# Kernel tuning notes

Measured on AMD Instinct MI355X. Metric: run time of the kernel, lower is better.

Reference implementation:

```python
import jax, jax.numpy as jnp
import numpy as np

C = 128

def setup_inputs() -> dict:
    key = jax.random.key(0)
    ks = jax.random.split(key, 7)
    s = 1.0 / np.sqrt(C)
    return {
        "x": jax.random.normal(ks[0], (8, C, 64, 64), dtype=jnp.float32),
        "Wq": jax.random.uniform(ks[1], (C, C), jnp.float32, -s, s),
        "bq": jax.random.uniform(ks[2], (C,), jnp.float32, -s, s),
        "Wk": jax.random.uniform(ks[3], (C, C), jnp.float32, -s, s),
        "bk": jax.random.uniform(ks[4], (C,), jnp.float32, -s, s),
        "Wv": jax.random.uniform(ks[5], (C, C), jnp.float32, -s, s),
        "bv": jax.random.uniform(ks[6], (C,), jnp.float32, -s, s),
    }

def reference(x, Wq, bq, Wk, bk, Wv, bv):
    bs, c, h, w = x.shape
    xf = x.reshape(bs, c, h * w)                      # [B, C, N]
    # 1x1 convs == per-pixel linear maps over channels
    q = jnp.einsum("dc,bcn->bdn", Wq, xf) + bq[None, :, None]
    k = jnp.einsum("dc,bcn->bdn", Wk, xf) + bk[None, :, None]
    v = jnp.einsum("dc,bcn->bdn", Wv, xf) + bv[None, :, None]
    # energy[b,i,j] = <q[:,i], k[:,j]>  (no 1/sqrt(d) scaling, per original)
    energy = jnp.einsum("bci,bcj->bij", q, k)         # [B, N, N]
    attn = jax.nn.softmax(energy, axis=-1)
    # out[b,c,i] = sum_j v[b,c,j] * attn[b,i,j]
    out = jnp.einsum("bcj,bij->bci", v, attn)
    return out.reshape(bs, c, h, w)
```

## Files before the change

### kernel.cpp

```cpp
#include <hip/hip_runtime.h>
#include <stdint.h>
#include <math.h>

typedef float  f32x4  __attribute__((ext_vector_type(4)));
typedef float  f32x16 __attribute__((ext_vector_type(16)));
typedef short  bf16x8 __attribute__((ext_vector_type(8)));
typedef unsigned int u32;
typedef unsigned int u32x4 __attribute__((ext_vector_type(4)));
typedef unsigned short ushort_t;

#define MFMA32(a, b, c) __builtin_amdgcn_mfma_f32_32x32x16_bf16((a), (b), (c), 0, 0, 0)

constexpr int B_ = 8, C_ = 128, N_ = 4096;
constexpr float LOG2E = 1.44269504088896340736f;

__device__ __forceinline__ u32 pack2bf(float a, float b) {
  u32 ua = __builtin_bit_cast(u32, a);
  u32 ub = __builtin_bit_cast(u32, b);
  ua += 0x7fffu + ((ua >> 16) & 1u);
  ub += 0x7fffu + ((ub >> 16) & 1u);
  return (ua >> 16) | (ub & 0xffff0000u);
}
__device__ __forceinline__ u32 pkfast(float a, float b) {
  u32 ua = __builtin_bit_cast(u32, a) + 0x8000u;
  u32 ub = __builtin_bit_cast(u32, b) + 0x8000u;
  return __builtin_amdgcn_perm(ub, ua, 0x07060302u);
}
__device__ __forceinline__ bf16x8 pack8(const float* v, float s) {
  u32x4 d = { pack2bf(v[0]*s, v[1]*s), pack2bf(v[2]*s, v[3]*s),
              pack2bf(v[4]*s, v[5]*s), pack2bf(v[6]*s, v[7]*s) };
  return __builtin_bit_cast(bf16x8, d);
}

__device__ __forceinline__ void gload_lds16(const ushort_t* g, ushort_t* l) {
  __builtin_amdgcn_global_load_lds(
      (const __attribute__((address_space(1))) void*)g,
      (__attribute__((address_space(3))) void*)l, 16, 0, 0);
}

__device__ __forceinline__ bf16x8 mk_pa(const f32x16& sv, int rb, float& lacc,
                                        int lq1) {
  float e0 = __builtin_amdgcn_exp2f(sv[rb+0]);
  float e1 = __builtin_amdgcn_exp2f(sv[rb+1]);
  float e2 = __builtin_amdgcn_exp2f(sv[rb+2]);
  float e3 = __builtin_amdgcn_exp2f(sv[rb+3]);
  float e4 = __builtin_amdgcn_exp2f(sv[rb+4]);
  float e5 = __builtin_amdgcn_exp2f(sv[rb+5]);
  float e6 = __builtin_amdgcn_exp2f(sv[rb+6]);
  float e7 = __builtin_amdgcn_exp2f(sv[rb+7]);
  lacc += ((e0+e1)+(e2+e3)) + ((e4+e5)+(e6+e7));
  u32 a  = pkfast(e0, e1), b2 = pkfast(e2, e3);
  u32 c2 = pkfast(e4, e5), d2 = pkfast(e6, e7);
  u32 s0v = lq1 ? a : c2;
  u32 s1v = lq1 ? b2 : d2;
  u32 r0 = __shfl_xor(s0v, 32);
  u32 r1 = __shfl_xor(s1v, 32);
  u32x4 fr;
  fr[0] = lq1 ? r0 : a;
  fr[1] = lq1 ? r1 : b2;
  fr[2] = lq1 ? c2 : r0;
  fr[3] = lq1 ? d2 : r1;
  return __builtin_bit_cast(bf16x8, fr);
}

__global__ __launch_bounds__(256)
void wprep_kernel(const float* __restrict__ Wq, const float* __restrict__ Wk,
                  const float* __restrict__ Wv, ushort_t* __restrict__ Wf)
{
  const int tid  = blockIdx.x * 256 + threadIdx.x;
  const int widx = tid >> 11;
  const int r    = tid & 2047;
  const int dt   = r >> 9;
  const int kc   = (r >> 6) & 7;
  const int ln   = r & 63;
  const float* W = (widx == 0) ? Wq : (widx == 1) ? Wk : Wv;
  const float s  = (widx == 0) ? LOG2E : 1.0f;
  const int d    = dt * 32 + (ln & 31);
  const int c0   = kc * 16 + (ln >> 5) * 8;
  const float* p = W + d * C_ + c0;
  f32x4 lo = *(const f32x4*)p, hi = *(const f32x4*)(p + 4);
  float v[8] = { lo.x, lo.y, lo.z, lo.w, hi.x, hi.y, hi.z, hi.w };
  *(bf16x8*)(Wf + (size_t)tid * 8) = pack8(v, s);
}

__global__ __launch_bounds__(256, 3)
void proj_kernel(const float* __restrict__ x,
                 const float* __restrict__ bq, const float* __restrict__ bk,
                 const float* __restrict__ bv, const ushort_t* __restrict__ Wf,
                 ushort_t* __restrict__ Qf, ushort_t* __restrict__ Kf,
                 ushort_t* __restrict__ Vf)
{
  const int b   = blockIdx.x & 7;
  const int nt  = blockIdx.x >> 3;
  const int n0  = nt << 5;
  const int t   = threadIdx.x;
  const int dt  = t >> 6;
  const int lane = t & 63;
  const int l31 = t & 31;
  const int lq1 = (t >> 5) & 1;

  __shared__ float xs[128 * 33];
  {
    const float* xb = x + (size_t)b * C_ * N_ + n0;
    const int m  = t & 7;
    const int cb = t >> 3;
#pragma unroll
    for (int it = 0; it < 4; ++it) {
      const int c = it * 32 + cb;
      f32x4 v = *(const f32x4*)(xb + (size_t)c * N_ + m * 4);
      *(f32x4*)&xs[c * 33 + m * 4] = v;
    }
  }
  __syncthreads();

  bf16x8 xf[8];
#pragma unroll
  for (int kc = 0; kc < 8; ++kc) {
    float v[8];
#pragma unroll
    for (int e = 0; e < 8; ++e)
      v[e] = xs[(kc * 16 + lq1 * 8 + e) * 33 + l31];
    xf[kc] = pack8(v, 1.0f);
  }

  const ushort_t* WQf = Wf;
  const ushort_t* WKf = Wf + 16384;
  const ushort_t* WVf = Wf + 32768;
  const f32x16 Z = {0,0,0,0,0,0,0,0,0,0,0,0,0,0,0,0};

  f32x16 sq = Z, sk = Z, sv = Z;
#pragma unroll
  for (int kc = 0; kc < 8; ++kc) {
    const size_t wo = (size_t)(dt * 8 + kc) * 512 + lane * 8;
    bf16x8 wq = *(const bf16x8*)(WQf + wo);
    bf16x8 wk = *(const bf16x8*)(WKf + wo);
    bf16x8 wvv = *(const bf16x8*)(WVf + wo);
    sq = MFMA32(wq, xf[kc], sq);
    sk = MFMA32(wk, xf[kc], sk);
    sv = MFMA32(xf[kc], wvv, sv);
  }

#pragma unroll
  for (int q = 0; q < 4; ++q) {
    const int dbase = dt * 32 + q * 8 + lq1 * 4;
    f32x4 b4q = *(const f32x4*)(bq + dbase);
    f32x4 b4k = *(const f32x4*)(bk + dbase);
    uint2 qs, ks;
    qs.x = pack2bf(sq[4*q+0] + b4q.x * LOG2E, sq[4*q+1] + b4q.y * LOG2E);
    qs.y = pack2bf(sq[4*q+2] + b4q.z * LOG2E, sq[4*q+3] + b4q.w * LOG2E);
    ks.x = pack2bf(sk[4*q+0] + b4k.x, sk[4*q+1] + b4k.y);
    ks.y = pack2bf(sk[4*q+2] + b4k.z, sk[4*q+3] + b4k.w);
    const int kcf = dt * 2 + (q >> 1), h = q & 1;
    const size_t off = ((size_t)((b * 128 + nt) * 8 + kcf) * 64 + h * 32 + l31) * 8 + lq1 * 4;
    *(uint2*)(Qf + off) = qs;
    *(uint2*)(Kf + off) = ks;
  }

  {
    const float bvl = bv[dt * 32 + l31];
    const int j64 = nt >> 1, qp = nt & 1;
#pragma unroll
    for (int q = 0; q < 4; ++q) {
      uint2 vs;
      vs.x = pack2bf(sv[4*q+0] + bvl, sv[4*q+1] + bvl);
      vs.y = pack2bf(sv[4*q+2] + bvl, sv[4*q+3] + bvl);
      const int cc = qp * 2 + (q >> 1);
      const size_t off = ((size_t)((b * 64 + j64) * 4 + dt) * 4 + cc) * 512 +
                         (size_t)((q & 1) * 32 + l31) * 8 + lq1 * 4;
      *(uint2*)(Vf + off) = vs;
    }
  }
}

__global__ __launch_bounds__(256, 3)
void flash_kernel(const ushort_t* __restrict__ Qf, const ushort_t* __restrict__ Kf,
                  const ushort_t* __restrict__ Vf, float* __restrict__ out,
                  float* __restrict__ opart, float* __restrict__ lpart, int js)
{
  const int b     = blockIdx.x & 7;
  const int itile = (blockIdx.x >> 3) & 31;
  const int jsl   = blockIdx.x >> 8;
  const int t     = threadIdx.x;
  const int wv    = t >> 6;
  const int lane  = t & 63;
  const int l31   = t & 31;
  const int lq1   = (t >> 5) & 1;
  const int i0    = itile * 128 + wv * 32;

  __shared__ __align__(16) short smem[16384];

  const int jt0 = (jsl * 128) / js;
  const int jt1 = ((jsl + 1) * 128) / js;
  const ushort_t* Kt0   = Kf + (size_t)b * 524288;
  const ushort_t* Vbase = Vf + (size_t)b * 524288;

  auto stage = [&](int jt, int p) {
    ushort_t* buf = (ushort_t*)smem + p * 8192;
    if (wv < 2) {
      const ushort_t* src = Kt0 + (size_t)jt * 4096;
#pragma unroll
      for (int c = 0; c < 4; ++c) {
        const int g = wv * 4 + c;
        gload_lds16(src + g * 512 + lane * 8, buf + g * 512);
      }
    } else {
      const int qp = jt & 1;
      const ushort_t* src = Vbase + (size_t)(jt >> 1) * 8192;
#pragma unroll
      for (int c = 0; c < 4; ++c) {
        const int h2 = (wv - 2) * 4 + c;
        const int ct = h2 >> 1, h = h2 & 1;
        gload_lds16(src + (size_t)(ct * 4 + qp * 2 + h) * 512 + lane * 8,
                    buf + 4096 + h2 * 512);
      }
    }
  };

  bf16x8 qf[8];
  const size_t qb = (size_t)((b * 128 + itile * 4 + wv) * 8) * 512;
#pragma unroll
  for (int kc = 0; kc < 8; ++kc)
    qf[kc] = *(const bf16x8*)(Qf + qb + (size_t)kc * 512 + lane * 8);

  const f32x16 Z = {0,0,0,0,0,0,0,0,0,0,0,0,0,0,0,0};
  f32x16 o[4] = {Z, Z, Z, Z};
  float lsum = 0.f;

  stage(jt0, 0);
  __syncthreads();

  for (int jt = jt0; jt < jt1; ++jt) {
    const int par = (jt - jt0) & 1;
    if (jt + 1 < jt1) stage(jt + 1, par ^ 1);

    const short* kbuf = smem + par * 8192;
    const short* vbuf = kbuf + 4096;

    f32x16 s = Z;
#pragma unroll
    for (int kc = 0; kc < 8; ++kc) {
      bf16x8 kf = *(const bf16x8*)&kbuf[kc * 512 + lane * 8];
      s = MFMA32(kf, qf[kc], s);
    }
    bf16x8 pa0 = mk_pa(s, 0, lsum, lq1);
    bf16x8 pa1 = mk_pa(s, 8, lsum, lq1);
#pragma unroll
    for (int ct = 0; ct < 4; ++ct) {
      bf16x8 vf0 = *(const bf16x8*)&vbuf[(ct * 2 + 0) * 512 + lane * 8];
      o[ct] = MFMA32(vf0, pa0, o[ct]);
      bf16x8 vf1 = *(const bf16x8*)&vbuf[(ct * 2 + 1) * 512 + lane * 8];
      o[ct] = MFMA32(vf1, pa1, o[ct]);
    }
    __syncthreads();
  }

  lsum += __shfl_xor(lsum, 32);
  const int ib = i0 + l31;

  if (js == 1) {
    const float inv = 1.0f / lsum;
#pragma unroll
    for (int ct = 0; ct < 4; ++ct)
#pragma unroll
      for (int rg = 0; rg < 16; ++rg) {
        const int c = ct * 32 + (rg >> 2) * 8 + lq1 * 4 + (rg & 3);
        out[(size_t)(b * C_ + c) * N_ + ib] = o[ct][rg] * inv;
      }
  } else {
    float* op = jsl ? (opart + (size_t)(jsl - 1) * B_ * C_ * N_) : out;
#pragma unroll
    for (int ct = 0; ct < 4; ++ct)
#pragma unroll
      for (int rg = 0; rg < 16; ++rg) {
        const int c = ct * 32 + (rg >> 2) * 8 + lq1 * 4 + (rg & 3);
        op[(size_t)(b * C_ + c) * N_ + ib] = o[ct][rg];
      }
    if (lane < 32)
      lpart[(size_t)jsl * B_ * N_ + (size_t)b * N_ + ib] = lsum;
  }
}

__global__ __launch_bounds__(256)
void combine_kernel(const float* __restrict__ opart, const float* __restrict__ lpart,
                    float* __restrict__ out, int js)
{
  const int t  = blockIdx.x * 256 + threadIdx.x;
  const int n4 = (t & 1023) * 4;
  const int bc = t >> 10;
  const int b  = bc >> 7;
  const size_t off  = (size_t)bc * N_ + n4;
  const size_t loff = (size_t)b * N_ + n4;
  f32x4 os = *(const f32x4*)(out + off);
  f32x4 ls = *(const f32x4*)(lpart + loff);
  for (int s = 1; s < js; ++s) {
    os += *(const f32x4*)(opart + (size_t)(s - 1) * B_ * C_ * N_ + off);
    ls += *(const f32x4*)(lpart + (size_t)s * B_ * N_ + loff);
  }
  f32x4 r = { os.x / ls.x, os.y / ls.y, os.z / ls.z, os.w / ls.w };
  *(f32x4*)(out + off) = r;
}

extern "C" void kernel_launch(void* const* d_in, const int* in_sizes, int n_in,
                              void* d_out, int out_size, void* d_ws, size_t ws_size,
                              hipStream_t stream) {
  const float* x  = (const float*)d_in[0];
  const float* Wq = (const float*)d_in[1];
  const float* bq = (const float*)d_in[2];
  const float* Wk = (const float*)d_in[3];
  const float* bk = (const float*)d_in[4];
  const float* Wv = (const float*)d_in[5];
  const float* bv = (const float*)d_in[6];
  float* out = (float*)d_out;

  const size_t nc = (size_t)B_ * N_ * C_;
  ushort_t* qf = (ushort_t*)d_ws;
  ushort_t* kf = qf + nc;
  ushort_t* vf = kf + nc;
  ushort_t* wf = vf + nc;
  const size_t base = (3 * nc + 49152) * sizeof(ushort_t);

  auto need = [&](int jss) {
    return base + (size_t)jss * (size_t)B_ * N_ * 4 +
           (size_t)(jss - 1) * (size_t)B_ * C_ * N_ * 4;
  };
  const int js = (ws_size >= need(3)) ? 3 : (ws_size >= need(2)) ? 2 : 1;

  float* lpart = (float*)((char*)d_ws + base);
  float* opart = lpart + (size_t)js * B_ * N_;

  hipLaunchKernelGGL(wprep_kernel, dim3(24), dim3(256), 0, stream, Wq, Wk, Wv, wf);
  hipLaunchKernelGGL(proj_kernel, dim3(1024), dim3(256), 0, stream,
                     x, bq, bk, bv, wf, qf, kf, vf);
  hipLaunchKernelGGL(flash_kernel, dim3(256 * js), dim3(256), 0, stream,
                     qf, kf, vf, out, opart, lpart, js);
  if (js > 1)
    hipLaunchKernelGGL(combine_kernel, dim3(4096), dim3(256), 0, stream,
                       opart, lpart, out, js);
}
```

Measured before the change: 173.9 us.

## Software-pipeline QK and PV across tiles with split K/V staging

Splits K and V staging into separate double buffers and restructures the main loop so the QK^T MFMAs for tile n+1 are issued alongside the PV MFMAs for tile n. The softmax exponentiation (mk_pa) then runs after both MFMA groups, so its VALU work can overlap with matrix-core work rather than sitting on the critical path between dependent MFMAs. It also raises wave priority around the MFMA block. In exchange it adds a prologue and epilogue, keeps more live registers (s plus pa0/pa1 across iterations), and staggers the K and V buffer indices in a way that must stay correct for every split count.

```diff
diff --git a/kernel.cpp b/kernel.cpp
--- a/kernel.cpp
+++ b/kernel.cpp
@@ -191,19 +191,24 @@
 
   const int jt0 = (jsl * 128) / js;
   const int jt1 = ((jsl + 1) * 128) / js;
+  const int NT  = jt1 - jt0;
   const ushort_t* Kt0   = Kf + (size_t)b * 524288;
   const ushort_t* Vbase = Vf + (size_t)b * 524288;
 
-  auto stage = [&](int jt, int p) {
-    ushort_t* buf = (ushort_t*)smem + p * 8192;
+  auto stageK = [&](int jt, int p) {
     if (wv < 2) {
+      ushort_t* buf = (ushort_t*)smem + p * 4096;
       const ushort_t* src = Kt0 + (size_t)jt * 4096;
 #pragma unroll
       for (int c = 0; c < 4; ++c) {
         const int g = wv * 4 + c;
         gload_lds16(src + g * 512 + lane * 8, buf + g * 512);
       }
-    } else {
+    }
+  };
+  auto stageV = [&](int jt, int p) {
+    if (wv >= 2) {
+      ushort_t* buf = (ushort_t*)smem + 8192 + p * 4096;
       const int qp = jt & 1;
       const ushort_t* src = Vbase + (size_t)(jt >> 1) * 8192;
 #pragma unroll
@@ -211,7 +216,7 @@
         const int h2 = (wv - 2) * 4 + c;
         const int ct = h2 >> 1, h = h2 & 1;
         gload_lds16(src + (size_t)(ct * 4 + qp * 2 + h) * 512 + lane * 8,
-                    buf + 4096 + h2 * 512);
+                    buf + h2 * 512);
       }
     }
   };
@@ -226,32 +231,51 @@
   f32x16 o[4] = {Z, Z, Z, Z};
   float lsum = 0.f;
 
-  stage(jt0, 0);
-  __syncthreads();
-
-  for (int jt = jt0; jt < jt1; ++jt) {
-    const int par = (jt - jt0) & 1;
-    if (jt + 1 < jt1) stage(jt + 1, par ^ 1);
-
-    const short* kbuf = smem + par * 8192;
-    const short* vbuf = kbuf + 4096;
-
+  auto qk = [&](const short* kbuf) -> f32x16 {
     f32x16 s = Z;
 #pragma unroll
     for (int kc = 0; kc < 8; ++kc) {
-      bf16x8 kf = *(const bf16x8*)&kbuf[kc * 512 + lane * 8];
-      s = MFMA32(kf, qf[kc], s);
-    }
-    bf16x8 pa0 = mk_pa(s, 0, lsum, lq1);
-    bf16x8 pa1 = mk_pa(s, 8, lsum, lq1);
+      bf16x8 kfr = *(const bf16x8*)&kbuf[kc * 512 + lane * 8];
+      s = MFMA32(kfr, qf[kc], s);
+    }
+    return s;
+  };
+  auto pv = [&](const short* vbuf, bf16x8 a0, bf16x8 a1) {
 #pragma unroll
     for (int ct = 0; ct < 4; ++ct) {
       bf16x8 vf0 = *(const bf16x8*)&vbuf[(ct * 2 + 0) * 512 + lane * 8];
-      o[ct] = MFMA32(vf0, pa0, o[ct]);
+      o[ct] = MFMA32(vf0, a0, o[ct]);
       bf16x8 vf1 = *(const bf16x8*)&vbuf[(ct * 2 + 1) * 512 + lane * 8];
-      o[ct] = MFMA32(vf1, pa1, o[ct]);
-    }
+      o[ct] = MFMA32(vf1, a1, o[ct]);
+    }
+  };
+
+  stageK(jt0, 0);
+  stageV(jt0, 0);
+  __syncthreads();
+  if (NT > 1) stageK(jt0 + 1, 1);
+  f32x16 s0 = qk(smem);
+  bf16x8 pa0 = mk_pa(s0, 0, lsum, lq1);
+  bf16x8 pa1 = mk_pa(s0, 8, lsum, lq1);
+  __syncthreads();
+
+  for (int n = 0; n < NT - 1; ++n) {
+    if (n + 2 < NT) stageK(jt0 + n + 2, n & 1);
+    stageV(jt0 + n + 1, (n + 1) & 1);
+    const short* kb = smem + ((n + 1) & 1) * 4096;
+    const short* vb = smem + 8192 + (n & 1) * 4096;
+    __builtin_amdgcn_s_setprio(1);
+    f32x16 s = qk(kb);
+    pv(vb, pa0, pa1);
+    __builtin_amdgcn_s_setprio(0);
+    pa0 = mk_pa(s, 0, lsum, lq1);
+    pa1 = mk_pa(s, 8, lsum, lq1);
     __syncthreads();
+  }
+
+  {
+    const short* vb = smem + 8192 + ((NT - 1) & 1) * 4096;
+    pv(vb, pa0, pa1);
   }
 
   lsum += __shfl_xor(lsum, 32);
```

After: 172.7 us. About the same (-0.7%).

## Triple-buffer K/V staging with all waves loading and explicit vmcnt waits

Applied to the files above, without the earlier changes.

Moves K/V LDS staging from double to triple buffering, keeping two tiles in flight ahead of compute. All four waves now share both K and V loads instead of splitting K to two waves and V to the other two. The full __syncthreads is replaced by a partial s_waitcnt vmcnt plus a raw s_barrier, so later loads stay outstanding across the barrier. MFMA sections are also wrapped in s_setprio. LDS use grows from 32KB to 48KB per block, which may limit the 3-blocks-per-CU occupancy target.

```diff
diff --git a/kernel.cpp b/kernel.cpp
--- a/kernel.cpp
+++ b/kernel.cpp
@@ -187,32 +187,31 @@
   const int lq1   = (t >> 5) & 1;
   const int i0    = itile * 128 + wv * 32;
 
-  __shared__ __align__(16) short smem[16384];
+  __shared__ __align__(16) short smem[24576];
 
   const int jt0 = (jsl * 128) / js;
   const int jt1 = ((jsl + 1) * 128) / js;
+  const int NT  = jt1 - jt0;
   const ushort_t* Kt0   = Kf + (size_t)b * 524288;
   const ushort_t* Vbase = Vf + (size_t)b * 524288;
 
   auto stage = [&](int jt, int p) {
-    ushort_t* buf = (ushort_t*)smem + p * 8192;
-    if (wv < 2) {
-      const ushort_t* src = Kt0 + (size_t)jt * 4096;
-#pragma unroll
-      for (int c = 0; c < 4; ++c) {
-        const int g = wv * 4 + c;
-        gload_lds16(src + g * 512 + lane * 8, buf + g * 512);
-      }
-    } else {
-      const int qp = jt & 1;
-      const ushort_t* src = Vbase + (size_t)(jt >> 1) * 8192;
-#pragma unroll
-      for (int c = 0; c < 4; ++c) {
-        const int h2 = (wv - 2) * 4 + c;
-        const int ct = h2 >> 1, h = h2 & 1;
-        gload_lds16(src + (size_t)(ct * 4 + qp * 2 + h) * 512 + lane * 8,
-                    buf + 4096 + h2 * 512);
-      }
+    ushort_t* kb = (ushort_t*)smem + p * 4096;
+    ushort_t* vb = (ushort_t*)smem + 12288 + p * 4096;
+    const ushort_t* ksrc = Kt0 + (size_t)jt * 4096;
+    const int qp = jt & 1;
+    const ushort_t* vsrc = Vbase + (size_t)(jt >> 1) * 8192;
+#pragma unroll
+    for (int c = 0; c < 2; ++c) {
+      const int g = wv * 2 + c;
+      gload_lds16(ksrc + g * 512 + lane * 8, kb + g * 512);
+    }
+#pragma unroll
+    for (int c = 0; c < 2; ++c) {
+      const int h2 = wv * 2 + c;
+      const int ct = h2 >> 1, h = h2 & 1;
+      gload_lds16(vsrc + (size_t)(ct * 4 + qp * 2 + h) * 512 + lane * 8,
+                  vb + h2 * 512);
     }
   };
 
@@ -226,32 +225,56 @@
   f32x16 o[4] = {Z, Z, Z, Z};
   float lsum = 0.f;
 
+  auto qk = [&](const short* kbuf) -> f32x16 {
+    f32x16 s = Z;
+#pragma unroll
+    for (int kc = 0; kc < 8; ++kc) {
+      bf16x8 kfr = *(const bf16x8*)&kbuf[kc * 512 + lane * 8];
+      s = MFMA32(kfr, qf[kc], s);
+    }
+    return s;
+  };
+  auto pv = [&](const short* vbuf, bf16x8 a0, bf16x8 a1) {
+#pragma unroll
+    for (int ct = 0; ct < 4; ++ct) {
+      bf16x8 vf0 = *(const bf16x8*)&vbuf[(ct * 2 + 0) * 512 + lane * 8];
+      o[ct] = MFMA32(vf0, a0, o[ct]);
+      bf16x8 vf1 = *(const bf16x8*)&vbuf[(ct * 2 + 1) * 512 + lane * 8];
+      o[ct] = MFMA32(vf1, a1, o[ct]);
+    }
+  };
+
   stage(jt0, 0);
-  __syncthreads();
-
-  for (int jt = jt0; jt < jt1; ++jt) {
-    const int par = (jt - jt0) & 1;
-    if (jt + 1 < jt1) stage(jt + 1, par ^ 1);
-
-    const short* kbuf = smem + par * 8192;
-    const short* vbuf = kbuf + 4096;
-
-    f32x16 s = Z;
-#pragma unroll
-    for (int kc = 0; kc < 8; ++kc) {
-      bf16x8 kf = *(const bf16x8*)&kbuf[kc * 512 + lane * 8];
-      s = MFMA32(kf, qf[kc], s);
-    }
+  stage(jt0 + 1, 1);
+  asm volatile("s_waitcnt vmcnt(4)" ::: "memory");
+  __builtin_amdgcn_sched_barrier(0);
+  __builtin_amdgcn_s_barrier();
+  __builtin_amdgcn_sched_barrier(0);
+
+  int pcur = 0, pstage = 2;
+  for (int n = 0; n < NT; ++n) {
+    if (n + 2 < NT) stage(jt0 + n + 2, pstage);
+    pstage = (pstage == 2) ? 0 : pstage + 1;
+    const short* kb = smem + pcur * 4096;
+    const short* vb = smem + 12288 + pcur * 4096;
+    pcur = (pcur == 2) ? 0 : pcur + 1;
+
+    __builtin_amdgcn_s_setprio(1);
+    f32x16 s = qk(kb);
+    __builtin_amdgcn_s_setprio(0);
     bf16x8 pa0 = mk_pa(s, 0, lsum, lq1);
     bf16x8 pa1 = mk_pa(s, 8, lsum, lq1);
-#pragma unroll
-    for (int ct = 0; ct < 4; ++ct) {
-      bf16x8 vf0 = *(const bf16x8*)&vbuf[(ct * 2 + 0) * 512 + lane * 8];
-      o[ct] = MFMA32(vf0, pa0, o[ct]);
-      bf16x8 vf1 = *(const bf16x8*)&vbuf[(ct * 2 + 1) * 512 + lane * 8];
-      o[ct] = MFMA32(vf1, pa1, o[ct]);
-    }
-    __syncthreads();
+    __builtin_amdgcn_s_setprio(1);
+    pv(vb, pa0, pa1);
+    __builtin_amdgcn_s_setprio(0);
+
+    if (n + 1 < NT) {
+      if (n + 2 < NT) asm volatile("s_waitcnt vmcnt(4)" ::: "memory");
+      else            asm volatile("s_waitcnt vmcnt(0)" ::: "memory");
+      __builtin_amdgcn_sched_barrier(0);
+      __builtin_amdgcn_s_barrier();
+      __builtin_amdgcn_sched_barrier(0);
+    }
   }
 
   lsum += __shfl_xor(lsum, 32);
```

Result: faster. 168.7 us (-3.0%).

## Load K/V tiles directly into registers, replace shuffles with permlane32 swap

Applied to the files above, without the earlier changes.

Drops the LDS double-buffered staging of K and V tiles in the flash kernel. Each wave now loads its K and V fragments straight from global memory into registers, with K software-pipelined one tile ahead, so no block-wide barrier is needed. The cross-half P fragment exchange uses v_permlane32_swap instead of two shfl_xor plus selects. Occupancy hint goes from 3 to 2 blocks per SM and the j-split goes from 3 to 2. The cost is redundant global/L2 traffic, since each wave reloads K/V that the LDS used to share across 4 waves, plus higher register pressure.

```diff
diff --git a/kernel.cpp b/kernel.cpp
--- a/kernel.cpp
+++ b/kernel.cpp
@@ -32,14 +32,7 @@
   return __builtin_bit_cast(bf16x8, d);
 }
 
-__device__ __forceinline__ void gload_lds16(const ushort_t* g, ushort_t* l) {
-  __builtin_amdgcn_global_load_lds(
-      (const __attribute__((address_space(1))) void*)g,
-      (__attribute__((address_space(3))) void*)l, 16, 0, 0);
-}
-
-__device__ __forceinline__ bf16x8 mk_pa(const f32x16& sv, int rb, float& lacc,
-                                        int lq1) {
+__device__ __forceinline__ bf16x8 mk_pa(const f32x16& sv, int rb, float& lacc) {
   float e0 = __builtin_amdgcn_exp2f(sv[rb+0]);
   float e1 = __builtin_amdgcn_exp2f(sv[rb+1]);
   float e2 = __builtin_amdgcn_exp2f(sv[rb+2]);
@@ -51,15 +44,9 @@
   lacc += ((e0+e1)+(e2+e3)) + ((e4+e5)+(e6+e7));
   u32 a  = pkfast(e0, e1), b2 = pkfast(e2, e3);
   u32 c2 = pkfast(e4, e5), d2 = pkfast(e6, e7);
-  u32 s0v = lq1 ? a : c2;
-  u32 s1v = lq1 ? b2 : d2;
-  u32 r0 = __shfl_xor(s0v, 32);
-  u32 r1 = __shfl_xor(s1v, 32);
-  u32x4 fr;
-  fr[0] = lq1 ? r0 : a;
-  fr[1] = lq1 ? r1 : b2;
-  fr[2] = lq1 ? c2 : r0;
-  fr[3] = lq1 ? d2 : r1;
+  asm("v_permlane32_swap_b32 %0, %1" : "+v"(a), "+v"(c2));
+  asm("v_permlane32_swap_b32 %0, %1" : "+v"(b2), "+v"(d2));
+  u32x4 fr = { a, b2, c2, d2 };
   return __builtin_bit_cast(bf16x8, fr);
 }
 
@@ -172,7 +159,7 @@
   }
 }
 
-__global__ __launch_bounds__(256, 3)
+__global__ __launch_bounds__(256, 2)
 void flash_kernel(const ushort_t* __restrict__ Qf, const ushort_t* __restrict__ Kf,
                   const ushort_t* __restrict__ Vf, float* __restrict__ out,
                   float* __restrict__ opart, float* __restrict__ lpart, int js)
@@ -187,35 +174,11 @@
   const int lq1   = (t >> 5) & 1;
   const int i0    = itile * 128 + wv * 32;
 
-  __shared__ __align__(16) short smem[16384];
-
   const int jt0 = (jsl * 128) / js;
   const int jt1 = ((jsl + 1) * 128) / js;
   const ushort_t* Kt0   = Kf + (size_t)b * 524288;
   const ushort_t* Vbase = Vf + (size_t)b * 524288;
 
-  auto stage = [&](int jt, int p) {
-    ushort_t* buf = (ushort_t*)smem + p * 8192;
-    if (wv < 2) {
-      const ushort_t* src = Kt0 + (size_t)jt * 4096;
-#pragma unroll
-      for (int c = 0; c < 4; ++c) {
-        const int g = wv * 4 + c;
-        gload_lds16(src + g * 512 + lane * 8, buf + g * 512);
-      }
-    } else {
-      const int qp = jt & 1;
-      const ushort_t* src = Vbase + (size_t)(jt >> 1) * 8192;
-#pragma unroll
-      for (int c = 0; c < 4; ++c) {
-        const int h2 = (wv - 2) * 4 + c;
-        const int ct = h2 >> 1, h = h2 & 1;
-        gload_lds16(src + (size_t)(ct * 4 + qp * 2 + h) * 512 + lane * 8,
-                    buf + 4096 + h2 * 512);
-      }
-    }
-  };
-
   bf16x8 qf[8];
   const size_t qb = (size_t)((b * 128 + itile * 4 + wv) * 8) * 512;
 #pragma unroll
@@ -226,32 +189,46 @@
   f32x16 o[4] = {Z, Z, Z, Z};
   float lsum = 0.f;
 
-  stage(jt0, 0);
-  __syncthreads();
-
-  for (int jt = jt0; jt < jt1; ++jt) {
-    const int par = (jt - jt0) & 1;
-    if (jt + 1 < jt1) stage(jt + 1, par ^ 1);
-
-    const short* kbuf = smem + par * 8192;
-    const short* vbuf = kbuf + 4096;
-
+  auto ldK = [&](int jt, bf16x8* kf) {
+    const ushort_t* src = Kt0 + (size_t)jt * 4096 + lane * 8;
+#pragma unroll
+    for (int kc = 0; kc < 8; ++kc)
+      kf[kc] = *(const bf16x8*)(src + kc * 512);
+  };
+
+  auto body = [&](const bf16x8* kf, int jt) {
     f32x16 s = Z;
 #pragma unroll
-    for (int kc = 0; kc < 8; ++kc) {
-      bf16x8 kf = *(const bf16x8*)&kbuf[kc * 512 + lane * 8];
-      s = MFMA32(kf, qf[kc], s);
-    }
-    bf16x8 pa0 = mk_pa(s, 0, lsum, lq1);
-    bf16x8 pa1 = mk_pa(s, 8, lsum, lq1);
+    for (int kc = 0; kc < 8; ++kc)
+      s = MFMA32(kf[kc], qf[kc], s);
+    bf16x8 vf[8];
+    {
+      const ushort_t* src = Vbase + (size_t)(jt >> 1) * 8192 +
+                            (size_t)(jt & 1) * 1024 + lane * 8;
+#pragma unroll
+      for (int ct = 0; ct < 4; ++ct) {
+        vf[ct*2+0] = *(const bf16x8*)(src + (ct*4+0) * 512);
+        vf[ct*2+1] = *(const bf16x8*)(src + (ct*4+1) * 512);
+      }
+    }
+    bf16x8 pa0 = mk_pa(s, 0, lsum);
+    bf16x8 pa1 = mk_pa(s, 8, lsum);
 #pragma unroll
     for (int ct = 0; ct < 4; ++ct) {
-      bf16x8 vf0 = *(const bf16x8*)&vbuf[(ct * 2 + 0) * 512 + lane * 8];
-      o[ct] = MFMA32(vf0, pa0, o[ct]);
-      bf16x8 vf1 = *(const bf16x8*)&vbuf[(ct * 2 + 1) * 512 + lane * 8];
-      o[ct] = MFMA32(vf1, pa1, o[ct]);
-    }
-    __syncthreads();
+      o[ct] = MFMA32(vf[ct*2+0], pa0, o[ct]);
+      o[ct] = MFMA32(vf[ct*2+1], pa1, o[ct]);
+    }
+  };
+
+  bf16x8 kfA[8], kfB[8];
+  ldK(jt0, kfA);
+  for (int n = jt0; n < jt1; n += 2) {
+    if (n + 1 < jt1) ldK(n + 1, kfB);
+    body(kfA, n);
+    if (n + 1 < jt1) {
+      if (n + 2 < jt1) ldK(n + 2, kfA);
+      body(kfB, n + 1);
+    }
   }
 
   lsum += __shfl_xor(lsum, 32);
@@ -323,7 +300,7 @@
     return base + (size_t)jss * (size_t)B_ * N_ * 4 +
            (size_t)(jss - 1) * (size_t)B_ * C_ * N_ * 4;
   };
-  const int js = (ws_size >= need(3)) ? 3 : (ws_size >= need(2)) ? 2 : 1;
+  const int js = (ws_size >= need(2)) ? 2 : 1;
 
   float* lpart = (float*)((char*)d_ws + base);
   float* opart = lpart + (size_t)js * B_ * N_;
```

Result: no change. 175.9 us (+1.1%).
